# Kernel tuning notes

Hardware: AMD Instinct MI355X
Metric: run time of the kernel (lower is better)

## Reference

```python
import jax, jax.numpy as jnp
import numpy as np

# Physiological constants (IHCPaulick2024 defaults, learnable=False)
FS = 44100.0                      # sampling rate [Hz]
SCALE = 10.0 ** (-105.0 / 20.0)   # stereocilia displacement scaling
GMET_MAX = 30e-9                  # max MET conductance [S]
X0 = 20e-9                        # displacement bias [m]
S0 = 16e-9                        # fast sensitivity [m]
S1 = 35e-9                        # slow sensitivity [m]
EP = 90e-3                        # endocochlear potential [V]
CM = 12.5e-12                     # membrane capacitance [F]
GKF = 19.8e-9                     # fast K+ conductance [S]
GKS = 19.8e-9                     # slow K+ conductance [S]
EKF = -71e-3                      # fast K+ reversal [V]
EKS = -78e-3                      # slow K+ reversal [V]
V_REST = -57.03e-3                # resting potential [V]
G_PRE = 3.3514e-9                 # pre-charge conductance [S]
PRE_DUR = 0.05                    # pre-charge duration [s]


def setup_inputs() -> dict:
    key = jax.random.key(0)
    # basilar-membrane velocity, shape (B, F, T)
    x = jax.random.normal(key, (8, 50, 131072), dtype=jnp.float32)
    return {"x": x}


def _precharge(dtype):
    """50 ms forward-Euler relaxation with fixed conductance -> steady-state V.
    Identical across (B, F) lanes, so computed as a scalar loop."""
    Ts = 1.0 / FS
    n_pre = int(FS * PRE_DUR)

    def step(_, v):
        Imet = G_PRE * (v - EP)
        Ik = GKF * (v - EKF)
        Is = GKS * (v - EKS)
        return v - (Imet + Ik + Is) * (Ts / CM)

    return jax.lax.fori_loop(0, n_pre, step, jnp.asarray(V_REST, dtype=dtype))


def reference(x):
    Ts = 1.0 / FS
    # 1) stereocilia displacement
    d = SCALE * x                                     # (B, F, T)
    # 2) MET channel conductance: double-exponential sigmoid
    z = X0 - d
    G = GMET_MAX / (1.0 + jnp.exp(z / S1) * (1.0 + jnp.exp(z / S0)))
    # 3) pre-charge to steady state
    v_pre = _precharge(x.dtype)                       # scalar
    V0 = jnp.full(x.shape[:2], v_pre, dtype=x.dtype)  # (B, F)
    # 4) forward-Euler membrane ODE over time (linear recurrence)
    Gt = jnp.moveaxis(G, -1, 0)                       # (T, B, F)

    def step(v, g_t):
        dv = (-g_t * (v - EP) - GKF * (v - EKF) - GKS * (v - EKS)) * (Ts / CM)
        v_new = v + dv
        return v_new, v_new

    _, Vs = jax.lax.scan(step, V0, Gt)                # (T, B, F)
    V = jnp.moveaxis(Vs, 0, -1)                       # (B, F, T)
    return V - v_pre
```

## Files before the change

kernel.cpp:

```cpp
#include <hip/hip_runtime.h>
#include <math.h>

static constexpr double dTS    = 1.0 / 44100.0;
static constexpr double dCM    = 12.5e-12;
static constexpr double dK     = dTS / dCM;
static constexpr double dGKF   = 19.8e-9;
static constexpr double dGKS   = 19.8e-9;
static constexpr double dEKF   = -71e-3;
static constexpr double dEKS   = -78e-3;
static constexpr double dEP    = 90e-3;
static constexpr double dGMET  = 30e-9;
static constexpr double dSCALE = 5.623413251903491e-06;
static constexpr double dX0    = 20e-9;
static constexpr double dS0    = 16e-9;
static constexpr double dS1    = 35e-9;
static constexpr double dL2E   = 1.4426950408889634;

static constexpr float F_K1   = (float)(-dSCALE / dS1 * dL2E);
static constexpr float F_C1   = (float)( dX0    / dS1 * dL2E);
static constexpr float F_K2   = (float)(-dSCALE * (1.0/dS1 + 1.0/dS0) * dL2E);
static constexpr float F_C2   = (float)( dX0    * (1.0/dS1 + 1.0/dS0) * dL2E);
static constexpr float F_ANOG = (float)(1.0 - (dGKF + dGKS) * dK);
static constexpr float F_GMK  = (float)(dGMET * dK);
static constexpr float F_EP   = (float)dEP;
static constexpr float F_C0   = (float)(dEP + (dGKF*(dEKF-dEP) + dGKS*(dEKS-dEP)) * dK);

constexpr int T_LEN = 131072;
constexpr int CHUNK = 8192;
constexpr int WARM  = 256;
constexpr int SPT   = 32;
constexpr int NTH   = 256;

typedef float v4f __attribute__((ext_vector_type(4)));

__device__ __forceinline__ float coef(float xv) {
    float e1  = __builtin_amdgcn_exp2f(fmaf(F_K1, xv, F_C1));
    float e2  = __builtin_amdgcn_exp2f(fmaf(F_K2, xv, F_C2));
    float den = 1.0f + e1 + e2;
    return fmaf(-F_GMK, __builtin_amdgcn_rcpf(den), F_ANOG);
}

__global__ __launch_bounds__(NTH, 5) void ihc_kernel(const float* __restrict__ x,
                                                     float* __restrict__ out,
                                                     float vpre) {
    const int c = blockIdx.x;
    const int l = blockIdx.y;
    const int t = threadIdx.x;
    const long lbase = (long)l * T_LEN;
    const float* xp  = x + lbase + (long)c * CHUNK;
    float* opc       = out + lbase + (long)c * CHUNK;

    __shared__ float lbuf[CHUNK];
    float4* lb4 = reinterpret_cast<float4*>(lbuf);

    float4 q[8];
    const float4* qp = reinterpret_cast<const float4*>(xp + t * SPT);
#pragma unroll
    for (int j = 0; j < 8; ++j) q[j] = qp[j];

    float aw, bw;
    {
        const int woff = (c == 0) ? 0 : -WARM;
        float wx = xp[t + woff];
        aw = coef(wx);
        bw = fmaf(-F_EP, aw, F_C0);
        if (c == 0) { aw = 1.0f; bw = 0.0f; }
    }

    float A = 1.0f, B = 0.0f;
#pragma unroll
    for (int j = 0; j < 8; ++j) {
        float ev[4] = {q[j].x, q[j].y, q[j].z, q[j].w};
#pragma unroll
        for (int i = 0; i < 4; ++i) {
            float a = coef(ev[i]);
            float b = fmaf(-F_EP, a, F_C0);
            B = fmaf(a, B, b);
            A = A * a;
            ev[i] = a;
        }
        q[j] = make_float4(ev[0], ev[1], ev[2], ev[3]);
    }

    const int lane = t & 63;
    const int w    = t >> 6;
#pragma unroll
    for (int d = 1; d < 64; d <<= 1) {
        float pa  = __shfl_up(A,  d, 64);
        float pb  = __shfl_up(B,  d, 64);
        float pwa = __shfl_up(aw, d, 64);
        float pwb = __shfl_up(bw, d, 64);
        if (lane >= d) {
            B  = fmaf(A,  pb,  B);  A  *= pa;
            bw = fmaf(aw, pwb, bw); aw *= pwa;
        }
    }

    if (lane == 63) {
        lbuf[w]      = aw;  lbuf[4 + w]  = bw;
        lbuf[8 + w]  = A;   lbuf[12 + w] = B;
    }
    __syncthreads();

    float wA = 1.0f, wB = 0.0f;
#pragma unroll
    for (int i = 0; i < 4; ++i) { wB = fmaf(lbuf[i], wB, lbuf[4 + i]); wA *= lbuf[i]; }
    float eA = 1.0f, eB = 0.0f;
    for (int i = 0; i < w; ++i) { eB = fmaf(lbuf[8 + i], eB, lbuf[12 + i]); eA *= lbuf[8 + i]; }
    float sa = __shfl_up(A, 1, 64);
    float sb = __shfl_up(B, 1, 64);
    if (lane == 0) { sa = 1.0f; sb = 0.0f; }

    float vw = fmaf(wA, vpre, wB);
    float u  = fmaf(eA, vw, eB);
    float v  = fmaf(sa, u, sb);
    __syncthreads();

    const int s = t & 7;
#pragma unroll
    for (int j = 0; j < 8; ++j) {
        float ev[4] = {q[j].x, q[j].y, q[j].z, q[j].w};
        float ov[4];
#pragma unroll
        for (int i = 0; i < 4; ++i) {
            float a = ev[i];
            float b = fmaf(-F_EP, a, F_C0);
            v = fmaf(a, v, b);
            ov[i] = v - vpre;
        }
        lb4[t * 8 + (j ^ s)] = make_float4(ov[0], ov[1], ov[2], ov[3]);
    }
    __syncthreads();

#pragma unroll
    for (int j = 0; j < 8; ++j) {
        int g  = t + NTH * j;
        int gp = g ^ ((g >> 3) & 7);
        float4 o = lb4[gp];
        v4f ov = { o.x, o.y, o.z, o.w };
        __builtin_nontemporal_store(ov, reinterpret_cast<v4f*>(opc + 4 * g));
    }
}

static float compute_vpre() {
    const float TsCM = (float)dK;
    float v = -57.03e-3f;
    for (int i = 0; i < 2205; ++i) {
        float Imet = 3.3514e-9f * (v - 0.09f);
        float Ik   = 19.8e-9f   * (v + 0.071f);
        float Is   = 19.8e-9f   * (v + 0.078f);
        v = v - (Imet + Ik + Is) * TsCM;
    }
    return v;
}

extern "C" void kernel_launch(void* const* d_in, const int* in_sizes, int n_in,
                              void* d_out, int out_size, void* d_ws, size_t ws_size,
                              hipStream_t stream) {
    const float* x = (const float*)d_in[0];
    float* out = (float*)d_out;
    const int lanes = in_sizes[0] / T_LEN;
    const int nchunks = T_LEN / CHUNK;
    float vpre = compute_vpre();
    dim3 grid(nchunks, lanes);
    hipLaunchKernelGGL(ihc_kernel, grid, dim3(NTH), 0, stream, x, out, vpre);
}
```

Baseline: 346.5 us.

## Process four consecutive segments per block with carried state and prefetch

```diff
diff --git a/kernel.cpp b/kernel.cpp
--- a/kernel.cpp
+++ b/kernel.cpp
@@ -26,12 +26,18 @@
 static constexpr float F_C0   = (float)(dEP + (dGKF*(dEKF-dEP) + dGKS*(dEKS-dEP)) * dK);
 
 constexpr int T_LEN = 131072;
-constexpr int CHUNK = 8192;
+constexpr int SEG   = 8192;
+constexpr int NSEG  = 4;
+constexpr int GROUP = SEG * NSEG;
 constexpr int WARM  = 256;
 constexpr int SPT   = 32;
 constexpr int NTH   = 256;
 
 typedef float v4f __attribute__((ext_vector_type(4)));
+
+__device__ __forceinline__ void bar_lds() {
+    asm volatile("s_waitcnt lgkmcnt(0)\n\ts_barrier" ::: "memory");
+}
 
 __device__ __forceinline__ float coef(float xv) {
     float e1  = __builtin_amdgcn_exp2f(fmaf(F_K1, xv, F_C1));
@@ -47,98 +53,130 @@
     const int l = blockIdx.y;
     const int t = threadIdx.x;
     const long lbase = (long)l * T_LEN;
-    const float* xp  = x + lbase + (long)c * CHUNK;
-    float* opc       = out + lbase + (long)c * CHUNK;
-
-    __shared__ float lbuf[CHUNK];
-    float4* lb4 = reinterpret_cast<float4*>(lbuf);
-
-    float4 q[8];
-    const float4* qp = reinterpret_cast<const float4*>(xp + t * SPT);
-#pragma unroll
-    for (int j = 0; j < 8; ++j) q[j] = qp[j];
-
-    float aw, bw;
-    {
-        const int woff = (c == 0) ? 0 : -WARM;
-        float wx = xp[t + woff];
-        aw = coef(wx);
-        bw = fmaf(-F_EP, aw, F_C0);
-        if (c == 0) { aw = 1.0f; bw = 0.0f; }
-    }
-
-    float A = 1.0f, B = 0.0f;
-#pragma unroll
-    for (int j = 0; j < 8; ++j) {
-        float ev[4] = {q[j].x, q[j].y, q[j].z, q[j].w};
-#pragma unroll
-        for (int i = 0; i < 4; ++i) {
-            float a = coef(ev[i]);
-            float b = fmaf(-F_EP, a, F_C0);
-            B = fmaf(a, B, b);
-            A = A * a;
-            ev[i] = a;
-        }
-        q[j] = make_float4(ev[0], ev[1], ev[2], ev[3]);
-    }
-
+    const float* xg = x + lbase + (long)c * GROUP;
+    float* og       = out + lbase + (long)c * GROUP;
     const int lane = t & 63;
     const int w    = t >> 6;
-#pragma unroll
-    for (int d = 1; d < 64; d <<= 1) {
-        float pa  = __shfl_up(A,  d, 64);
-        float pb  = __shfl_up(B,  d, 64);
-        float pwa = __shfl_up(aw, d, 64);
-        float pwb = __shfl_up(bw, d, 64);
-        if (lane >= d) {
-            B  = fmaf(A,  pb,  B);  A  *= pa;
-            bw = fmaf(aw, pwb, bw); aw *= pwa;
-        }
+    const int s7   = t & 7;
+
+    __shared__ float lbuf[SEG];
+    float4* lb4 = reinterpret_cast<float4*>(lbuf);
+
+    float4 q[8];
+    {
+        const float4* qp = reinterpret_cast<const float4*>(xg + t * SPT);
+#pragma unroll
+        for (int j = 0; j < 8; ++j) q[j] = qp[j];
     }
-
-    if (lane == 63) {
-        lbuf[w]      = aw;  lbuf[4 + w]  = bw;
-        lbuf[8 + w]  = A;   lbuf[12 + w] = B;
-    }
-    __syncthreads();
-
-    float wA = 1.0f, wB = 0.0f;
-#pragma unroll
-    for (int i = 0; i < 4; ++i) { wB = fmaf(lbuf[i], wB, lbuf[4 + i]); wA *= lbuf[i]; }
-    float eA = 1.0f, eB = 0.0f;
-    for (int i = 0; i < w; ++i) { eB = fmaf(lbuf[8 + i], eB, lbuf[12 + i]); eA *= lbuf[8 + i]; }
-    float sa = __shfl_up(A, 1, 64);
-    float sb = __shfl_up(B, 1, 64);
-    if (lane == 0) { sa = 1.0f; sb = 0.0f; }
-
-    float vw = fmaf(wA, vpre, wB);
-    float u  = fmaf(eA, vw, eB);
-    float v  = fmaf(sa, u, sb);
-    __syncthreads();
-
-    const int s = t & 7;
-#pragma unroll
-    for (int j = 0; j < 8; ++j) {
-        float ev[4] = {q[j].x, q[j].y, q[j].z, q[j].w};
-        float ov[4];
-#pragma unroll
-        for (int i = 0; i < 4; ++i) {
-            float a = ev[i];
-            float b = fmaf(-F_EP, a, F_C0);
-            v = fmaf(a, v, b);
-            ov[i] = v - vpre;
-        }
-        lb4[t * 8 + (j ^ s)] = make_float4(ov[0], ov[1], ov[2], ov[3]);
-    }
-    __syncthreads();
-
-#pragma unroll
-    for (int j = 0; j < 8; ++j) {
-        int g  = t + NTH * j;
-        int gp = g ^ ((g >> 3) & 7);
-        float4 o = lb4[gp];
-        v4f ov = { o.x, o.y, o.z, o.w };
-        __builtin_nontemporal_store(ov, reinterpret_cast<v4f*>(opc + 4 * g));
+    const float wx = xg[t + ((c == 0) ? 0 : -WARM)];
+    float aw = coef(wx);
+    float bw = fmaf(-F_EP, aw, F_C0);
+    if (c == 0) { aw = 1.0f; bw = 0.0f; }
+
+    float vseg = vpre;
+
+#pragma unroll
+    for (int s = 0; s < NSEG; ++s) {
+        float4 qn[8];
+        if (s < NSEG - 1) {
+            const float4* qp = reinterpret_cast<const float4*>(xg + (s + 1) * SEG + t * SPT);
+#pragma unroll
+            for (int j = 0; j < 8; ++j) qn[j] = qp[j];
+        }
+
+        float A = 1.0f, B = 0.0f;
+#pragma unroll
+        for (int j = 0; j < 8; ++j) {
+            float ev[4] = {q[j].x, q[j].y, q[j].z, q[j].w};
+#pragma unroll
+            for (int i = 0; i < 4; ++i) {
+                float a = coef(ev[i]);
+                float b = fmaf(-F_EP, a, F_C0);
+                B = fmaf(a, B, b);
+                A = A * a;
+                ev[i] = a;
+            }
+            q[j] = make_float4(ev[0], ev[1], ev[2], ev[3]);
+        }
+
+        if (s == 0) {
+#pragma unroll
+            for (int d = 1; d < 64; d <<= 1) {
+                float pa  = __shfl_up(A,  d, 64);
+                float pb  = __shfl_up(B,  d, 64);
+                float pwa = __shfl_up(aw, d, 64);
+                float pwb = __shfl_up(bw, d, 64);
+                if (lane >= d) {
+                    B  = fmaf(A,  pb,  B);  A  *= pa;
+                    bw = fmaf(aw, pwb, bw); aw *= pwa;
+                }
+            }
+        } else {
+#pragma unroll
+            for (int d = 1; d < 64; d <<= 1) {
+                float pa = __shfl_up(A, d, 64);
+                float pb = __shfl_up(B, d, 64);
+                if (lane >= d) { B = fmaf(A, pb, B); A *= pa; }
+            }
+        }
+
+        bar_lds();
+        if (lane == 63) {
+            if (s == 0) { lbuf[w] = aw; lbuf[4 + w] = bw; }
+            lbuf[8 + w] = A; lbuf[12 + w] = B;
+        }
+        bar_lds();
+
+        float wA = 1.0f, wB = 0.0f;
+        if (s == 0) {
+#pragma unroll
+            for (int i = 0; i < 4; ++i) { wB = fmaf(lbuf[i], wB, lbuf[4 + i]); wA *= lbuf[i]; }
+        }
+        float eA = 1.0f, eB = 0.0f;
+        for (int i = 0; i < w; ++i) { eB = fmaf(lbuf[8 + i], eB, lbuf[12 + i]); eA *= lbuf[8 + i]; }
+        float At = eA, Bt = eB;
+        for (int i = w; i < 4; ++i) { Bt = fmaf(lbuf[8 + i], Bt, lbuf[12 + i]); At *= lbuf[8 + i]; }
+
+        float sa = __shfl_up(A, 1, 64);
+        float sb = __shfl_up(B, 1, 64);
+        if (lane == 0) { sa = 1.0f; sb = 0.0f; }
+
+        const float vw = (s == 0) ? fmaf(wA, vseg, wB) : vseg;
+        float u = fmaf(eA, vw, eB);
+        float v = fmaf(sa, u, sb);
+        vseg = fmaf(At, vw, Bt);
+
+        bar_lds();
+
+#pragma unroll
+        for (int j = 0; j < 8; ++j) {
+            float ev[4] = {q[j].x, q[j].y, q[j].z, q[j].w};
+            float ov[4];
+#pragma unroll
+            for (int i = 0; i < 4; ++i) {
+                float a = ev[i];
+                float b = fmaf(-F_EP, a, F_C0);
+                v = fmaf(a, v, b);
+                ov[i] = v - vpre;
+            }
+            lb4[t * 8 + (j ^ s7)] = make_float4(ov[0], ov[1], ov[2], ov[3]);
+        }
+        bar_lds();
+
+        float* ops = og + s * SEG;
+#pragma unroll
+        for (int j = 0; j < 8; ++j) {
+            int g  = t + NTH * j;
+            int gp = g ^ ((g >> 3) & 7);
+            float4 o = lb4[gp];
+            v4f ov = { o.x, o.y, o.z, o.w };
+            __builtin_nontemporal_store(ov, reinterpret_cast<v4f*>(ops + 4 * g));
+        }
+
+        if (s < NSEG - 1) {
+#pragma unroll
+            for (int j = 0; j < 8; ++j) q[j] = qn[j];
+        }
     }
 }
 
@@ -160,8 +198,8 @@
     const float* x = (const float*)d_in[0];
     float* out = (float*)d_out;
     const int lanes = in_sizes[0] / T_LEN;
-    const int nchunks = T_LEN / CHUNK;
+    const int ngroups = T_LEN / GROUP;
     float vpre = compute_vpre();
-    dim3 grid(nchunks, lanes);
+    dim3 grid(ngroups, lanes);
     hipLaunchKernelGGL(ihc_kernel, grid, dim3(NTH), 0, stream, x, out, vpre);
 }
```

Result: slower. 421.3 us (+21.6%).
